# Performance work log

Hardware: AMD Instinct MI355X
Metric: run time of the kernel (lower is better)

## Reference

```python
import jax, jax.numpy as jnp
import numpy as np

NEG = -1.0e30  # finite stand-in for -inf (NaN-safe under autodiff)


def rnnt_loss_mean(logits, ys, ylen):
    # logits: (B, T, U+1, V); ys: (B, U) int labels; ylen: (B,) label lengths.
    # blank index = 0; per the original forward, xlen == T for every batch element.
    lp = jax.nn.log_softmax(logits, axis=-1)
    lp_blank = lp[..., 0]  # (B, T, U1)
    # lp_label[b, t, u] = lp[b, t, u, ys[b, u]]  for u < U
    lp_label = jnp.take_along_axis(
        lp[:, :, :-1, :], ys[:, None, :, None].astype(jnp.int32), axis=3
    )[..., 0]  # (B, T, U)
    B, T, U1 = lp_blank.shape
    # emit[b, t, u] = lp_label[b, t, u-1], with emit[..., 0] = -inf
    emit = jnp.concatenate([jnp.full((B, T, 1), NEG, lp.dtype), lp_label], axis=2)
    # alpha[0, u] = sum_{k<u} lp_label[b, 0, k]
    row0 = jnp.concatenate(
        [jnp.zeros((B, 1), lp.dtype), jnp.cumsum(lp_label[:, 0, :], axis=1)], axis=1
    )  # (B, U1)

    def u_step(carry, au_eu):
        a_u, e_u = au_eu  # each (B,)
        new = jnp.logaddexp(a_u, carry + e_u)
        return new, new

    def t_step(prev_row, inp):
        blank_prev, emit_t = inp  # each (B, U1)
        a = prev_row + blank_prev  # horizontal (time) move
        init = jnp.full((B,), NEG, lp.dtype)
        _, new_row = jax.lax.scan(u_step, init, (a.T, emit_t.T))  # (U1, B)
        return new_row.T, None

    last_row, _ = jax.lax.scan(
        t_step,
        row0,
        (jnp.swapaxes(lp_blank[:, :-1, :], 0, 1), jnp.swapaxes(emit[:, 1:, :], 0, 1)),
    )  # (B, U1) = alpha[T-1, :]
    yl = ylen[:, None].astype(jnp.int32)
    alpha_end = jnp.take_along_axis(last_row, yl, axis=1)[:, 0]
    blank_end = jnp.take_along_axis(lp_blank[:, T - 1, :], yl, axis=1)[:, 0]
    return jnp.mean(-(alpha_end + blank_end))


def setup_inputs():
    B, T, U, H, V = 8, 200, 50, 320, 1024
    key = jax.random.key(0)
    ks = jax.random.split(key, 12)
    s = np.float32(1.0 / np.sqrt(H))
    return {
        "encoder_output": jax.random.normal(ks[0], (B, T, H), jnp.float32),
        "prediction_output": jax.random.normal(ks[1], (B, U + 1, H), jnp.float32),
        "xs": jax.random.normal(ks[2], (B, T, 80), jnp.float32),  # unused by forward
        "xlen": jnp.full((B,), T, jnp.int32),  # overwritten to T in original code
        "ys": jax.random.randint(ks[3], (B, U), 1, V, dtype=jnp.int32),
        "ylen": jax.random.randint(ks[4], (B,), 1, U + 1, dtype=jnp.int32),
        "W_enc": jax.random.normal(ks[5], (H, H), jnp.float32) * s,
        "b_enc": jnp.zeros((H,), jnp.float32),
        "W_pred": jax.random.normal(ks[6], (H, H), jnp.float32) * s,
        "b_pred": jnp.zeros((H,), jnp.float32),
        "W_ff_enc": jax.random.normal(ks[7], (H, V), jnp.float32) * s,
        "W_ff_pred": jax.random.normal(ks[8], (H, V), jnp.float32) * s,
        "b_ff": jnp.zeros((V,), jnp.float32),
    }


def reference(encoder_output, prediction_output, xs, xlen, ys, ylen,
              W_enc, b_enc, W_pred, b_pred, W_ff_enc, W_ff_pred, b_ff):
    # linear_enc / linear_pred commute with the broadcast-expand, so apply them first.
    enc_proj = encoder_output @ W_enc + b_enc        # (B, T, H)
    pred_proj = prediction_output @ W_pred + b_pred  # (B, U1, H)
    # cat + linear_feed_forward == split-weight matmuls summed over the broadcast.
    enc_part = enc_proj @ W_ff_enc    # (B, T, V)
    pred_part = pred_proj @ W_ff_pred  # (B, U1, V)
    logits = enc_part[:, :, None, :] + pred_part[:, None, :, :] + b_ff  # (B, T, U1, V)
    loss = rnnt_loss_mean(logits, ys, ylen)
    return loss, logits
```

## Files before the change

kernel.cpp:

```cpp
#include <hip/hip_runtime.h>
#include <hip/hip_bf16.h>
#include <cstddef>

#define Bdim 8
#define Tdim 200
#define Udim 50
#define U1dim 51
#define Hdim 320
#define Vdim 1024
#define NEGV -1.0e30f
#define LOG2E 1.4426950408889634f
#define LN2f  0.6931471805599453f

using short8 = __attribute__((ext_vector_type(8))) short;
using f32x4  = __attribute__((ext_vector_type(4))) float;

static __device__ __forceinline__ ushort f2bf(float x) {
    __hip_bfloat16 h = __float2bfloat16(x);
    return *reinterpret_cast<ushort*>(&h);
}
static __device__ __forceinline__ int pack2(float a, float b) {
    return (int)f2bf(a) | ((int)f2bf(b) << 16);
}

__global__ __launch_bounds__(256) void fuse_weights(
    const float* __restrict__ W_enc, const float* __restrict__ W_ff_enc,
    const float* __restrict__ W_pred, const float* __restrict__ W_ff_pred,
    const float* __restrict__ b_enc, const float* __restrict__ b_pred,
    const float* __restrict__ b_ff,
    ushort* __restrict__ Wfe_t, ushort* __restrict__ Wfp_t,
    float* __restrict__ cvec, float* __restrict__ dvec)
{
    const int tid = threadIdx.x;
    if (blockIdx.y == 16) {
        if (blockIdx.x > 1) return;
        const bool e = (blockIdx.x == 0);
        const float* bv = e ? b_enc : b_pred;
        const float* Wf = e ? W_ff_enc : W_ff_pred;
        float* ovec = e ? cvec : dvec;
        const int v = tid * 4;
        float4 acc = make_float4(0.f, 0.f, 0.f, 0.f);
        for (int p = 0; p < Hdim; ++p) {
            float s = bv[p];
            float4 w = *(const float4*)&Wf[(size_t)p * Vdim + v];
            acc.x += s * w.x; acc.y += s * w.y; acc.z += s * w.z; acc.w += s * w.w;
        }
        if (e) {
            float4 bf = *(const float4*)&b_ff[v];
            acc.x += bf.x; acc.y += bf.y; acc.z += bf.z; acc.w += bf.w;
        }
        *(float4*)&ovec[v] = acc;
        return;
    }

    const bool e = (blockIdx.x < 5);
    const float* A  = e ? W_ff_enc : W_ff_pred;
    const float* Bm = e ? W_enc    : W_pred;
    ushort* Cout    = e ? Wfe_t    : Wfp_t;
    const int n0 = (blockIdx.x % 5) * 64;
    const int m0 = blockIdx.y * 64;

    __shared__ short As[64][40];
    __shared__ short Bs[64][40];

    const int ar = tid >> 3;
    const int ac = (tid & 7) * 8;
    const int br = tid >> 2;
    const int bc = (tid & 3) * 8;

    const int lane = tid & 63;
    const int wave = tid >> 6;
    const int wr = wave >> 1, wc = wave & 1;
    const int lrow = lane & 15;
    const int kg = (lane >> 4) * 8;

    f32x4 acc[2][2] = {};

    for (int k0 = 0; k0 < Hdim; k0 += 32) {
        float4 a0 = *(const float4*)&A[(size_t)(k0 + ar) * Vdim + m0 + ac];
        float4 a1 = *(const float4*)&A[(size_t)(k0 + ar) * Vdim + m0 + ac + 4];
        As[ac + 0][ar] = (short)f2bf(a0.x);
        As[ac + 1][ar] = (short)f2bf(a0.y);
        As[ac + 2][ar] = (short)f2bf(a0.z);
        As[ac + 3][ar] = (short)f2bf(a0.w);
        As[ac + 4][ar] = (short)f2bf(a1.x);
        As[ac + 5][ar] = (short)f2bf(a1.y);
        As[ac + 6][ar] = (short)f2bf(a1.z);
        As[ac + 7][ar] = (short)f2bf(a1.w);
        float4 w0 = *(const float4*)&Bm[(size_t)(n0 + br) * Hdim + k0 + bc];
        float4 w1 = *(const float4*)&Bm[(size_t)(n0 + br) * Hdim + k0 + bc + 4];
        int4 bp = make_int4(pack2(w0.x, w0.y), pack2(w0.z, w0.w),
                            pack2(w1.x, w1.y), pack2(w1.z, w1.w));
        *(int4*)&Bs[br][bc] = bp;
        __syncthreads();

        short8 fa0 = *(const short8*)&As[wr * 32 + lrow][kg];
        short8 fa1 = *(const short8*)&As[wr * 32 + 16 + lrow][kg];
        short8 fb0 = *(const short8*)&Bs[wc * 32 + lrow][kg];
        short8 fb1 = *(const short8*)&Bs[wc * 32 + 16 + lrow][kg];
        acc[0][0] = __builtin_amdgcn_mfma_f32_16x16x32_bf16(fa0, fb0, acc[0][0], 0, 0, 0);
        acc[0][1] = __builtin_amdgcn_mfma_f32_16x16x32_bf16(fa0, fb1, acc[0][1], 0, 0, 0);
        acc[1][0] = __builtin_amdgcn_mfma_f32_16x16x32_bf16(fa1, fb0, acc[1][0], 0, 0, 0);
        acc[1][1] = __builtin_amdgcn_mfma_f32_16x16x32_bf16(fa1, fb1, acc[1][1], 0, 0, 0);
        __syncthreads();
    }

    #pragma unroll
    for (int fm = 0; fm < 2; ++fm) {
        #pragma unroll
        for (int fn = 0; fn < 2; ++fn) {
            int col = n0 + wc * 32 + fn * 16 + lrow;
            int r0 = m0 + wr * 32 + fm * 16 + (lane >> 4) * 4;
            #pragma unroll
            for (int r = 0; r < 4; ++r)
                Cout[(size_t)(r0 + r) * Hdim + col] = f2bf(acc[fm][fn][r]);
        }
    }
}

__global__ __launch_bounds__(256) void main_gemm(
    const float* __restrict__ enc, const float* __restrict__ pred,
    const ushort* __restrict__ Wfe_t, const ushort* __restrict__ Wfp_t,
    const float* __restrict__ cvec, const float* __restrict__ dvec,
    float* __restrict__ enc_part, float* __restrict__ pred_part)
{
    const bool e = (blockIdx.y < 25);
    const float*  A    = e ? enc : pred;
    const ushort* Bt   = e ? Wfe_t : Wfp_t;
    const float*  bias = e ? cvec : dvec;
    float*        C    = e ? enc_part : pred_part;
    const int M  = e ? (Bdim * Tdim) : (Bdim * U1dim);
    const int m0 = (e ? blockIdx.y : blockIdx.y - 25) * 64;
    const int n0 = blockIdx.x * 64;

    __shared__ short As[64][40];
    __shared__ short Bs[64][40];
    const int tid = threadIdx.x;
    const int sr = tid >> 2;
    const int sc = (tid & 3) * 8;

    const int lane = tid & 63;
    const int wave = tid >> 6;
    const int wr = wave >> 1, wc = wave & 1;
    const int lrow = lane & 15;
    const int kg = (lane >> 4) * 8;

    f32x4 acc[2][2] = {};

    for (int k0 = 0; k0 < Hdim; k0 += 32) {
        int4 av = make_int4(0, 0, 0, 0);
        if (m0 + sr < M) {
            float4 x0 = *(const float4*)&A[(size_t)(m0 + sr) * Hdim + k0 + sc];
            float4 x1 = *(const float4*)&A[(size_t)(m0 + sr) * Hdim + k0 + sc + 4];
            av = make_int4(pack2(x0.x, x0.y), pack2(x0.z, x0.w),
                           pack2(x1.x, x1.y), pack2(x1.z, x1.w));
        }
        *(int4*)&As[sr][sc] = av;
        *(int4*)&Bs[sr][sc] = *(const int4*)&Bt[(size_t)(n0 + sr) * Hdim + k0 + sc];
        __syncthreads();

        short8 fa0 = *(const short8*)&As[wr * 32 + lrow][kg];
        short8 fa1 = *(const short8*)&As[wr * 32 + 16 + lrow][kg];
        short8 fb0 = *(const short8*)&Bs[wc * 32 + lrow][kg];
        short8 fb1 = *(const short8*)&Bs[wc * 32 + 16 + lrow][kg];
        acc[0][0] = __builtin_amdgcn_mfma_f32_16x16x32_bf16(fa0, fb0, acc[0][0], 0, 0, 0);
        acc[0][1] = __builtin_amdgcn_mfma_f32_16x16x32_bf16(fa0, fb1, acc[0][1], 0, 0, 0);
        acc[1][0] = __builtin_amdgcn_mfma_f32_16x16x32_bf16(fa1, fb0, acc[1][0], 0, 0, 0);
        acc[1][1] = __builtin_amdgcn_mfma_f32_16x16x32_bf16(fa1, fb1, acc[1][1], 0, 0, 0);
        __syncthreads();
    }

    #pragma unroll
    for (int fm = 0; fm < 2; ++fm) {
        #pragma unroll
        for (int fn = 0; fn < 2; ++fn) {
            int col = n0 + wc * 32 + fn * 16 + lrow;
            int r0 = m0 + wr * 32 + fm * 16 + (lane >> 4) * 4;
            float bv = bias[col];
            #pragma unroll
            for (int r = 0; r < 4; ++r) {
                int row = r0 + r;
                if (row < M)
                    C[(size_t)row * Vdim + col] = acc[fm][fn][r] + bv;
            }
        }
    }
}

__global__ __launch_bounds__(256) void joint_lse(
    const float* __restrict__ enc_part, const float* __restrict__ pred_part,
    const int* __restrict__ ys, float* __restrict__ out,
    float* __restrict__ lp_blank, float* __restrict__ lp_label)
{
    const int b = blockIdx.x;
    const int chunk = blockIdx.y;
    const int tid = threadIdx.x;
    const int lane = tid & 63;
    const int wave = tid >> 6;
    if (b == 0 && chunk == 0 && tid == 0) out[0] = 0.f;
    const int t0 = chunk * 16 + wave * 4;
    if (t0 >= Tdim) return;

    float4 e0[4], e1[4], e2[4], e3[4];
    #pragma unroll
    for (int j = 0; j < 4; ++j) {
        const float* Erow = enc_part + (size_t)(b * Tdim + t0 + j) * Vdim + lane * 16;
        e0[j] = *(const float4*)(Erow + 0);
        e1[j] = *(const float4*)(Erow + 4);
        e2[j] = *(const float4*)(Erow + 8);
        e3[j] = *(const float4*)(Erow + 12);
    }

    const float* Pbase = pred_part + (size_t)b * U1dim * Vdim + lane * 16;
    float* logits = out + 1;

    float4 p0, p1, p2, p3;
    {
        const float* P = Pbase;
        p0 = *(const float4*)(P + 0);
        p1 = *(const float4*)(P + 4);
        p2 = *(const float4*)(P + 8);
        p3 = *(const float4*)(P + 12);
    }

    for (int u = 0; u < U1dim; ++u) {
        float4 q0, q1, q2, q3;
        if (u + 1 < U1dim) {
            const float* P = Pbase + (size_t)(u + 1) * Vdim;
            q0 = *(const float4*)(P + 0);
            q1 = *(const float4*)(P + 4);
            q2 = *(const float4*)(P + 8);
            q3 = *(const float4*)(P + 12);
        }

        const int vlab = (u < Udim) ? ys[b * Udim + u] : 0;
        const int idx = vlab & 15;
        const int src = vlab >> 4;

        #pragma unroll
        for (int j = 0; j < 4; ++j) {
            float xa[16];
            xa[0] = e0[j].x + p0.x;  xa[1] = e0[j].y + p0.y;
            xa[2] = e0[j].z + p0.z;  xa[3] = e0[j].w + p0.w;
            xa[4] = e1[j].x + p1.x;  xa[5] = e1[j].y + p1.y;
            xa[6] = e1[j].z + p1.z;  xa[7] = e1[j].w + p1.w;
            xa[8] = e2[j].x + p2.x;  xa[9] = e2[j].y + p2.y;
            xa[10]= e2[j].z + p2.z;  xa[11]= e2[j].w + p2.w;
            xa[12]= e3[j].x + p3.x;  xa[13]= e3[j].y + p3.y;
            xa[14]= e3[j].z + p3.z;  xa[15]= e3[j].w + p3.w;

            float nx0 = __shfl_down(xa[0], 1);
            float nx1 = __shfl_down(xa[1], 1);
            float nx2 = __shfl_down(xa[2], 1);

            const int bt = b * Tdim + t0 + j;
            float* rowb = logits + ((size_t)bt * U1dim + u) * Vdim;
            float* W = rowb + 3 + lane * 16;
            *(float4*)(W + 0) = make_float4(xa[3],  xa[4],  xa[5],  xa[6]);
            *(float4*)(W + 4) = make_float4(xa[7],  xa[8],  xa[9],  xa[10]);
            *(float4*)(W + 8) = make_float4(xa[11], xa[12], xa[13], xa[14]);
            if (lane < 63) {
                *(float4*)(W + 12) = make_float4(xa[15], nx0, nx1, nx2);
            } else {
                rowb[1023] = xa[15];
            }
            if (lane == 0) {
                rowb[0] = xa[0];
                rowb[1] = xa[1];
                rowb[2] = xa[2];
            }

            float s = 0.f;
            #pragma unroll
            for (int i = 0; i < 16; ++i) s += __expf(xa[i]);
            #pragma unroll
            for (int off = 32; off >= 1; off >>= 1) s += __shfl_xor(s, off);
            float lse = __logf(s);

            float cand = xa[0];
            #pragma unroll
            for (int i = 1; i < 16; ++i) if (i == idx) cand = xa[i];
            float lab = __shfl(cand, src);

            if (lane == 0) {
                lp_blank[(size_t)bt * U1dim + u] = xa[0] - lse;
                if (u < Udim) lp_label[(size_t)bt * Udim + u] = lab - lse;
            }
        }

        p0 = q0; p1 = q1; p2 = q2; p3 = q3;
    }
}

__global__ __launch_bounds__(256) void alpha_kernel(
    const float* __restrict__ lp_blank, const float* __restrict__ lp_label,
    const int* __restrict__ ylen, float* __restrict__ out)
{
    __shared__ float s_bl[U1dim * Tdim];
    __shared__ float s_lab[Udim * Tdim];
    const int b = blockIdx.x;
    const int tid = threadIdx.x;
    const float* gb = lp_blank + (size_t)b * Tdim * U1dim;
    const float* gl = lp_label + (size_t)b * Tdim * Udim;
    for (int i = tid; i < Tdim * U1dim; i += 256) {
        int t = i / U1dim, u = i % U1dim;
        s_bl[u * Tdim + t] = gb[i] * LOG2E;
    }
    for (int i = tid; i < Tdim * Udim; i += 256) {
        int t = i / Udim, u = i % Udim;
        s_lab[u * Tdim + t] = gl[i] * LOG2E;
    }
    __syncthreads();

    if (tid < 64) {
        const int u = tid;
        float cur = NEGV;
        for (int d = 0; d < Tdim + U1dim - 1; ++d) {
            float left = __shfl_up(cur, 1);
            int t = d - u;
            if (u < U1dim && t >= 0 && t < Tdim) {
                float h = (t >= 1) ? cur + s_bl[u * Tdim + (t - 1)] : NEGV;
                float g = (u >= 1) ? left + s_lab[(u - 1) * Tdim + t] : NEGV;
                float mx = fmaxf(h, g);
                float nv = mx + __log2f(1.0f + exp2f(-fabsf(h - g)));
                if (d == 0) nv = 0.f;
                cur = nv;
            }
        }
        const int L = ylen[b];
        if (u == L)
            atomicAdd(out, -(cur + s_bl[L * Tdim + (Tdim - 1)]) * (LN2f / Bdim));
    }
}

extern "C" void kernel_launch(void* const* d_in, const int* in_sizes, int n_in,
                              void* d_out, int out_size, void* d_ws, size_t ws_size,
                              hipStream_t stream)
{
    const float* enc      = (const float*)d_in[0];
    const float* pred     = (const float*)d_in[1];
    const int*   ys       = (const int*)d_in[4];
    const int*   ylen     = (const int*)d_in[5];
    const float* W_enc    = (const float*)d_in[6];
    const float* b_enc    = (const float*)d_in[7];
    const float* W_pred   = (const float*)d_in[8];
    const float* b_pred   = (const float*)d_in[9];
    const float* W_ff_enc = (const float*)d_in[10];
    const float* W_ff_pred= (const float*)d_in[11];
    const float* b_ff     = (const float*)d_in[12];
    float* out = (float*)d_out;
    char* ws = (char*)d_ws;

    float*  enc_part  = (float*) (ws + 0);
    float*  pred_part = (float*) (ws + 6553600);
    ushort* Wfe_t     = (ushort*)(ws + 8224768);
    ushort* Wfp_t     = (ushort*)(ws + 8880128);
    float*  cvec      = (float*) (ws + 9535488);
    float*  dvec      = (float*) (ws + 9539584);
    float*  lp_blank  = (float*) (ws + 9543680);
    float*  lp_label  = (float*) (ws + 9870080);

    dim3 blk(256);
    fuse_weights<<<dim3(10, 17), blk, 0, stream>>>(
        W_enc, W_ff_enc, W_pred, W_ff_pred, b_enc, b_pred, b_ff,
        Wfe_t, Wfp_t, cvec, dvec);
    main_gemm<<<dim3(16, 32), blk, 0, stream>>>(
        enc, pred, Wfe_t, Wfp_t, cvec, dvec, enc_part, pred_part);
    joint_lse<<<dim3(Bdim, 13), blk, 0, stream>>>(
        enc_part, pred_part, ys, out, lp_blank, lp_label);
    alpha_kernel<<<dim3(Bdim), blk, 0, stream>>>(lp_blank, lp_label, ylen, out);
}
```

Before: 222.8 us.

## Split logits write into separate high-parallelism kernel from log-prob computation

Moves the large logits materialization out of the joint log-softmax kernel into a new logits_kernel launched with a wider grid (8x50 blocks, one time step per wave). The lp kernel now only computes blank/label log-probs, so the serial alpha kernel gets its inputs sooner. The intent is to spread the memory-bound logits store across many more blocks and CUs than the 8x13 grid allowed. The cost is that enc_part and pred_part are read a second time.

```diff
diff --git a/kernel.cpp b/kernel.cpp
--- a/kernel.cpp
+++ b/kernel.cpp
@@ -187,7 +187,7 @@
     }
 }
 
-__global__ __launch_bounds__(256) void joint_lse(
+__global__ __launch_bounds__(256) void lp_kernel(
     const float* __restrict__ enc_part, const float* __restrict__ pred_part,
     const int* __restrict__ ys, float* __restrict__ out,
     float* __restrict__ lp_blank, float* __restrict__ lp_label)
@@ -212,26 +212,13 @@
     }
 
     const float* Pbase = pred_part + (size_t)b * U1dim * Vdim + lane * 16;
-    float* logits = out + 1;
-
-    float4 p0, p1, p2, p3;
-    {
-        const float* P = Pbase;
-        p0 = *(const float4*)(P + 0);
-        p1 = *(const float4*)(P + 4);
-        p2 = *(const float4*)(P + 8);
-        p3 = *(const float4*)(P + 12);
-    }
 
     for (int u = 0; u < U1dim; ++u) {
-        float4 q0, q1, q2, q3;
-        if (u + 1 < U1dim) {
-            const float* P = Pbase + (size_t)(u + 1) * Vdim;
-            q0 = *(const float4*)(P + 0);
-            q1 = *(const float4*)(P + 4);
-            q2 = *(const float4*)(P + 8);
-            q3 = *(const float4*)(P + 12);
-        }
+        const float* P = Pbase + (size_t)u * Vdim;
+        float4 p0 = *(const float4*)(P + 0);
+        float4 p1 = *(const float4*)(P + 4);
+        float4 p2 = *(const float4*)(P + 8);
+        float4 p3 = *(const float4*)(P + 12);
 
         const int vlab = (u < Udim) ? ys[b * Udim + u] : 0;
         const int idx = vlab & 15;
@@ -249,27 +236,6 @@
             xa[12]= e3[j].x + p3.x;  xa[13]= e3[j].y + p3.y;
             xa[14]= e3[j].z + p3.z;  xa[15]= e3[j].w + p3.w;
 
-            float nx0 = __shfl_down(xa[0], 1);
-            float nx1 = __shfl_down(xa[1], 1);
-            float nx2 = __shfl_down(xa[2], 1);
-
-            const int bt = b * Tdim + t0 + j;
-            float* rowb = logits + ((size_t)bt * U1dim + u) * Vdim;
-            float* W = rowb + 3 + lane * 16;
-            *(float4*)(W + 0) = make_float4(xa[3],  xa[4],  xa[5],  xa[6]);
-            *(float4*)(W + 4) = make_float4(xa[7],  xa[8],  xa[9],  xa[10]);
-            *(float4*)(W + 8) = make_float4(xa[11], xa[12], xa[13], xa[14]);
-            if (lane < 63) {
-                *(float4*)(W + 12) = make_float4(xa[15], nx0, nx1, nx2);
-            } else {
-                rowb[1023] = xa[15];
-            }
-            if (lane == 0) {
-                rowb[0] = xa[0];
-                rowb[1] = xa[1];
-                rowb[2] = xa[2];
-            }
-
             float s = 0.f;
             #pragma unroll
             for (int i = 0; i < 16; ++i) s += __expf(xa[i]);
@@ -283,9 +249,77 @@
             float lab = __shfl(cand, src);
 
             if (lane == 0) {
+                const int bt = b * Tdim + t0 + j;
                 lp_blank[(size_t)bt * U1dim + u] = xa[0] - lse;
                 if (u < Udim) lp_label[(size_t)bt * Udim + u] = lab - lse;
             }
+        }
+    }
+}
+
+__global__ __launch_bounds__(256) void logits_kernel(
+    const float* __restrict__ enc_part, const float* __restrict__ pred_part,
+    float* __restrict__ out)
+{
+    const int b = blockIdx.x;
+    const int chunk = blockIdx.y;
+    const int tid = threadIdx.x;
+    const int lane = tid & 63;
+    const int wave = tid >> 6;
+    const int t = chunk * 4 + wave;
+    const int bt = b * Tdim + t;
+
+    const float* Erow = enc_part + (size_t)bt * Vdim + lane * 16;
+    float4 e0 = *(const float4*)(Erow + 0);
+    float4 e1 = *(const float4*)(Erow + 4);
+    float4 e2 = *(const float4*)(Erow + 8);
+    float4 e3 = *(const float4*)(Erow + 12);
+
+    const float* Pbase = pred_part + (size_t)b * U1dim * Vdim + lane * 16;
+    float* region = out + 1 + (size_t)bt * U1dim * Vdim;
+
+    float4 p0, p1, p2, p3;
+    {
+        p0 = *(const float4*)(Pbase + 0);
+        p1 = *(const float4*)(Pbase + 4);
+        p2 = *(const float4*)(Pbase + 8);
+        p3 = *(const float4*)(Pbase + 12);
+    }
+
+    for (int u = 0; u < U1dim; ++u) {
+        float4 q0, q1, q2, q3;
+        if (u + 1 < U1dim) {
+            const float* P = Pbase + (size_t)(u + 1) * Vdim;
+            q0 = *(const float4*)(P + 0);
+            q1 = *(const float4*)(P + 4);
+            q2 = *(const float4*)(P + 8);
+            q3 = *(const float4*)(P + 12);
+        }
+
+        float xa[16];
+        xa[0]=e0.x+p0.x;  xa[1]=e0.y+p0.y;  xa[2]=e0.z+p0.z;  xa[3]=e0.w+p0.w;
+        xa[4]=e1.x+p1.x;  xa[5]=e1.y+p1.y;  xa[6]=e1.z+p1.z;  xa[7]=e1.w+p1.w;
+        xa[8]=e2.x+p2.x;  xa[9]=e2.y+p2.y;  xa[10]=e2.z+p2.z; xa[11]=e2.w+p2.w;
+        xa[12]=e3.x+p3.x; xa[13]=e3.y+p3.y; xa[14]=e3.z+p3.z; xa[15]=e3.w+p3.w;
+
+        float nx0 = __shfl_down(xa[0], 1);
+        float nx1 = __shfl_down(xa[1], 1);
+        float nx2 = __shfl_down(xa[2], 1);
+
+        float* rowb = region + (size_t)u * Vdim;
+        float* W = rowb + 3 + lane * 16;
+        *(float4*)(W + 0) = make_float4(xa[3],  xa[4],  xa[5],  xa[6]);
+        *(float4*)(W + 4) = make_float4(xa[7],  xa[8],  xa[9],  xa[10]);
+        *(float4*)(W + 8) = make_float4(xa[11], xa[12], xa[13], xa[14]);
+        if (lane < 63) {
+            *(float4*)(W + 12) = make_float4(xa[15], nx0, nx1, nx2);
+        } else {
+            rowb[1023] = xa[15];
+        }
+        if (lane == 0) {
+            rowb[0] = xa[0];
+            rowb[1] = xa[1];
+            rowb[2] = xa[2];
         }
 
         p0 = q0; p1 = q1; p2 = q2; p3 = q3;
@@ -366,7 +400,9 @@
         Wfe_t, Wfp_t, cvec, dvec);
     main_gemm<<<dim3(16, 32), blk, 0, stream>>>(
         enc, pred, Wfe_t, Wfp_t, cvec, dvec, enc_part, pred_part);
-    joint_lse<<<dim3(Bdim, 13), blk, 0, stream>>>(
+    lp_kernel<<<dim3(Bdim, 13), blk, 0, stream>>>(
         enc_part, pred_part, ys, out, lp_blank, lp_label);
     alpha_kernel<<<dim3(Bdim), blk, 0, stream>>>(lp_blank, lp_label, ylen, out);
-}
+    logits_kernel<<<dim3(Bdim, 50), blk, 0, stream>>>(
+        enc_part, pred_part, out);
+}
```

After: 277.1 us. 1.24x slower.
